# Kernel optimization log

Hardware: AMD Instinct MI355X
Metric: run time of the kernel (lower is better)

Reference implementation:

```python
import jax, jax.numpy as jnp
import numpy as np

KS, PAD = 3, 1  # AttentionConv kernel_size=3, padding=1, stride=1, groups=1


def _unfold(t, H, W):
    # t: [B, C, H+2*PAD, W+2*PAD] -> [B, C, H, W, KS*KS] local windows
    return jnp.stack([t[:, :, i:i + H, j:j + W]
                      for i in range(KS) for j in range(KS)], axis=-1)


def _attn_conv(x, wq, bq, wk, bk, wv, bv, rh, rw):
    # SASA local self-attention conv. x: [B, Cin, H, W]; wq/wk/wv: [Cout, Cin]
    B, Cin, H, W = x.shape
    q = jnp.einsum('bchw,oc->bohw', x, wq) + bq[None, :, None, None]
    xp = jnp.pad(x, ((0, 0), (0, 0), (PAD, PAD), (PAD, PAD)))
    k = jnp.einsum('bchw,oc->bohw', xp, wk) + bk[None, :, None, None]
    v = jnp.einsum('bchw,oc->bohw', xp, wv) + bv[None, :, None, None]
    k = _unfold(k, H, W)  # [B, Cout, H, W, 9]
    v = _unfold(v, H, W)
    Ch = rh.shape[0]  # Cout // 2
    # relative embeddings: first channel half gets rel_h (varies along kh),
    # second half gets rel_w (varies along kw)
    rel = jnp.concatenate([
        jnp.broadcast_to(rh[:, :, None], (Ch, KS, KS)),
        jnp.broadcast_to(rw[:, None, :], (Ch, KS, KS)),
    ], axis=0).reshape(2 * Ch, KS * KS)
    k = k + rel[None, :, None, None, :]
    attn = jax.nn.softmax(q[..., None] * k, axis=-1)  # per-channel softmax over window
    return jnp.einsum('bchwk,bchwk->bchw', attn, v)


def setup_inputs() -> dict:
    key = jax.random.key(0)
    ks = jax.random.split(key, 16)
    B, Cin, Cout = 4, 256, 512
    S, F, O = 64500, 489, 140
    inp = {
        'p3': jax.random.normal(ks[0], (B, Cin, 64, 64), jnp.float32),
        'p4': jax.random.normal(ks[1], (B, Cin, 32, 32), jnp.float32),
        'p5': jax.random.normal(ks[2], (B, Cin, 16, 16), jnp.float32),
        'wq': jax.random.normal(ks[3], (3, Cout, Cin), jnp.float32) * 0.01,
        'bq': jnp.zeros((3, Cout), jnp.float32),
        'wk': jax.random.normal(ks[4], (3, Cout, Cin), jnp.float32) * 0.01,
        'bk': jnp.zeros((3, Cout), jnp.float32),
        'wv': jax.random.normal(ks[5], (3, Cout, Cin), jnp.float32) * 0.01,
        'bv': jnp.zeros((3, Cout), jnp.float32),
        'rel_h': jax.random.normal(ks[6], (3, Cout // 2, KS), jnp.float32),
        'rel_w': jax.random.normal(ks[7], (3, Cout // 2, KS), jnp.float32),
        'ws': jax.random.normal(ks[8], (S, Cout), jnp.float32) * 0.01,
        'bs': jnp.zeros((S,), jnp.float32),
        'wf': jax.random.normal(ks[9], (F, Cout), jnp.float32) * 0.01,
        'bf': jnp.zeros((F,), jnp.float32),
        'wo': jax.random.normal(ks[10], (O, Cout), jnp.float32) * 0.01,
        'bo': jnp.zeros((O,), jnp.float32),
    }
    return inp


def reference(p3, p4, p5, wq, bq, wk, bk, wv, bv, rel_h, rel_w,
              ws, bs, wf, bf, wo, bo):
    feat = 0.
    for i, x in enumerate((p3, p4, p5)):
        y = _attn_conv(x, wq[i], bq[i], wk[i], bk[i], wv[i], bv[i],
                       rel_h[i], rel_w[i])
        y = jax.nn.relu(y)
        feat = feat + y.mean(axis=(2, 3))  # AdaptiveAvgPool2d((1,1)) -> [B, 512]
    # 1x1 conv classifiers on [B, 512, 1, 1] == dense layers; .view(N, -1)
    logits_species = feat @ ws.T + bs
    logits_family = feat @ wf.T + bf
    logits_order = feat @ wo.T + bo
    return (logits_species, logits_family, logits_order)
```

## Files before the change

### kernel.cpp

```cpp
#include <hip/hip_runtime.h>
#include <hip/hip_bf16.h>
#include <stdint.h>

typedef __bf16 bf16x8 __attribute__((ext_vector_type(8)));
typedef float  f32x4  __attribute__((ext_vector_type(4)));
typedef unsigned short u16x8 __attribute__((ext_vector_type(8)));
typedef unsigned int   u32x4 __attribute__((ext_vector_type(4)));

__device__ __forceinline__ unsigned short f2bf(float f) {
    union { float f; unsigned u; } v; v.f = f;
    unsigned r = v.u + 0x7fffu + ((v.u >> 16) & 1u);
    return (unsigned short)(r >> 16);
}
__device__ __forceinline__ float bf2f(unsigned short u) {
    union { unsigned u; float f; } v; v.u = (unsigned)u << 16; return v.f;
}
__device__ __forceinline__ float lo16(unsigned d) {
    union { unsigned u; float f; } v; v.u = d << 16; return v.f;
}
__device__ __forceinline__ float hi16(unsigned d) {
    union { unsigned u; float f; } v; v.u = d & 0xffff0000u; return v.f;
}
__device__ __forceinline__ float fexp2(float x) {
    float r; asm("v_exp_f32 %0, %1" : "=v"(r) : "v"(x)); return r;
}
__device__ __forceinline__ float frcp(float x) {
    float r; asm("v_rcp_f32 %0, %1" : "=v"(r) : "v"(x)); return r;
}

__device__ __forceinline__ void async16(void* lds, const void* g) {
    __builtin_amdgcn_global_load_lds(
        (const __attribute__((address_space(1))) unsigned int*)g,
        (__attribute__((address_space(3))) unsigned int*)lds, 16, 0, 0);
}

#define NT_ALL   21504
#define OFF_L1   16384
#define OFF_L2   20480

__global__ __launch_bounds__(256) void prep_kernel(
    const float* __restrict__ x0, const float* __restrict__ x1,
    const float* __restrict__ x2,
    const float* __restrict__ wq, const float* __restrict__ wk,
    const float* __restrict__ wv,
    unsigned short* __restrict__ wb, unsigned short* __restrict__ xT,
    float* __restrict__ feat)
{
    __shared__ unsigned short tile[64][65];
    int bid = blockIdx.x;
    if (bid == 0) {
        for (int i = threadIdx.x; i < 2048; i += 256) feat[i] = 0.f;
        return;
    }
    bid -= 1;
    if (bid < 576) {
        int t = bid / 192;
        int i = ((bid % 192) * 256 + threadIdx.x) * 8;
        const float* src = (t == 0) ? wq : (t == 1) ? wk : wv;
        f32x4 a = *(const f32x4*)(src + i);
        f32x4 b = *(const f32x4*)(src + i + 4);
        u16x8 o;
        o[0] = f2bf(a.x); o[1] = f2bf(a.y); o[2] = f2bf(a.z); o[3] = f2bf(a.w);
        o[4] = f2bf(b.x); o[5] = f2bf(b.y); o[6] = f2bf(b.z); o[7] = f2bf(b.w);
        *(u16x8*)(wb + (size_t)t * 393216 + i) = o;
        return;
    }
    bid -= 576;
    int xb = bid % 84;
    int c0 = ((bid / 84) & 3) * 64;
    int b  = bid / 336;
    const float* xp; int tb, HW, lvl_off;
    if (xb < 64)      { xp = x0; tb = xb;      HW = 4096; lvl_off = 0;      }
    else if (xb < 80) { xp = x1; tb = xb - 64; HW = 1024; lvl_off = OFF_L1; }
    else              { xp = x2; tb = xb - 80; HW = 256;  lvl_off = OFF_L2; }
    int hw0 = tb * 64;
    xp += (size_t)b * 256 * HW;
    int tx = threadIdx.x & 63;
    int ty = threadIdx.x >> 6;
#pragma unroll
    for (int i = 0; i < 16; ++i) {
        int c = c0 + ty * 16 + i;
        tile[ty * 16 + i][tx] = f2bf(xp[(size_t)c * HW + hw0 + tx]);
    }
    __syncthreads();
    unsigned short* op = xT + ((size_t)lvl_off + (size_t)b * HW + hw0) * 256 + c0;
#pragma unroll
    for (int i = 0; i < 16; ++i) {
        int r = ty * 16 + i;
        op[(size_t)r * 256 + tx] = tile[tx][r];
    }
}

__global__ __launch_bounds__(256, 2) void qkv_gemm_kernel(
    const unsigned short* __restrict__ wb,
    const float* __restrict__ bq, const float* __restrict__ bk,
    const float* __restrict__ bv,
    const unsigned short* __restrict__ xT,
    unsigned short* __restrict__ qkv)
{
    int bid = blockIdx.x;
    int swz = (bid & 7) * 252 + (bid >> 3);
    int nt  = swz / 12;
    int mz  = swz % 12;
    int z   = mz >> 2;
    int bm0 = (mz & 3) * 128;
    int bn0 = nt * 128;
    int lvl = (bn0 >= OFF_L2) ? 2 : (bn0 >= OFF_L1) ? 1 : 0;
    const unsigned short* Wm = wb + ((size_t)z * 3 + lvl) * 131072;
    const float* bias = ((z == 0) ? bq : (z == 1) ? bk : bv) + lvl * 512;
    unsigned short* out = qkv + (size_t)z * 512 * NT_ALL;

    __shared__ unsigned short smem[2][8192];

    int tid  = threadIdx.x;
    int lane = tid & 63;
    int wid  = tid >> 6;
    int wr   = wid >> 1, wc = wid & 1;
    int l15  = lane & 15;
    int kg   = lane >> 4;

    f32x4 acc[4][4];
#pragma unroll
    for (int i = 0; i < 4; ++i)
#pragma unroll
        for (int j = 0; j < 4; ++j) acc[i][j] = (f32x4){0.f, 0.f, 0.f, 0.f};

    int aRow0 = bm0 + (2 * wid)     * 16 + l15;
    int aRow1 = bm0 + (2 * wid + 1) * 16 + l15;
    int bRow0 = bn0 + (2 * wid)     * 16 + l15;
    int bRow1 = bn0 + (2 * wid + 1) * 16 + l15;
    int kbase = kg * 8;

    auto STAGE = [&](int t, int bufi) {
        int kk = t * 32 + kbase;
        unsigned short* As = smem[bufi];
        unsigned short* Bs = As + 4096;
        async16(As + (2 * wid)     * 512, Wm + (size_t)aRow0 * 256 + kk);
        async16(As + (2 * wid + 1) * 512, Wm + (size_t)aRow1 * 256 + kk);
        async16(Bs + (2 * wid)     * 512, xT + (size_t)bRow0 * 256 + kk);
        async16(Bs + (2 * wid + 1) * 512, xT + (size_t)bRow1 * 256 + kk);
    };

    STAGE(0, 0);
    __syncthreads();

    for (int it = 0; it < 8; ++it) {
        if (it < 7) STAGE(it + 1, (it + 1) & 1);
        const unsigned short* As = smem[it & 1];
        const unsigned short* Bs = As + 4096;
        bf16x8 af[4], bg[4];
#pragma unroll
        for (int mi = 0; mi < 4; ++mi)
            af[mi] = *reinterpret_cast<const bf16x8*>(As + ((wr * 4 + mi) * 64 + lane) * 8);
#pragma unroll
        for (int ni = 0; ni < 4; ++ni)
            bg[ni] = *reinterpret_cast<const bf16x8*>(Bs + ((wc * 4 + ni) * 64 + lane) * 8);
#pragma unroll
        for (int mi = 0; mi < 4; ++mi)
#pragma unroll
            for (int ni = 0; ni < 4; ++ni)
                acc[mi][ni] = __builtin_amdgcn_mfma_f32_16x16x32_bf16(
                    af[mi], bg[ni], acc[mi][ni], 0, 0, 0);
        __syncthreads();
    }

    unsigned short* T = smem[0];
#pragma unroll
    for (int p = 0; p < 2; ++p) {
        __syncthreads();
#pragma unroll
        for (int s = 0; s < 2; ++s) {
            int mi = 2 * p + s;
            int qw = wr * 32 + s * 16 + kg * 4;
            int ow = bm0 + wr * 64 + mi * 16 + kg * 4;
#pragma unroll
            for (int ni = 0; ni < 4; ++ni) {
                int cn = wc * 64 + ni * 16 + l15;
#pragma unroll
                for (int r = 0; r < 4; ++r)
                    T[(qw + r) * 136 + cn] = f2bf(acc[mi][ni][r] + bias[ow + r]);
            }
        }
        __syncthreads();
        int q  = tid >> 2;
        int j4 = tid & 3;
        int o  = bm0 + (q >> 5) * 64 + (2 * p + ((q >> 4) & 1)) * 16 + (q & 15);
        unsigned short* orow = out + (size_t)o * NT_ALL + bn0;
#pragma unroll
        for (int c = 0; c < 4; ++c) {
            int nl = c * 32 + j4 * 8;
            *(u16x8*)(orow + nl) = *(const u16x8*)(T + q * 136 + nl);
        }
    }
}

__global__ __launch_bounds__(256, 4) void attn_kernel(
    const unsigned short* __restrict__ qkv,
    const float* __restrict__ bk, const float* __restrict__ bv,
    const float* __restrict__ relh, const float* __restrict__ relw,
    float* __restrict__ feat)
{
    int xb = blockIdx.x;
    int c  = blockIdx.y;
    int lvl, lgW, lvl_off, hw_all;
    if (xb < 8)       { lvl = 0; lgW = 6; lvl_off = 0;      hw_all = xb * 2048 + threadIdx.x * 8; }
    else if (xb < 10) { lvl = 1; lgW = 5; lvl_off = OFF_L1; hw_all = (xb - 8) * 2048 + threadIdx.x * 8; }
    else              { lvl = 2; lgW = 4; lvl_off = OFF_L2; hw_all = threadIdx.x * 8; }
    int W = 1 << lgW, H = W, HW = W << lgW;
    bool active = hw_all < 4 * HW;
    int b  = hw_all >> (2 * lgW);
    int hw = hw_all & (HW - 1);
    int h = hw >> lgW, w0 = hw & (W - 1);

    size_t n0 = (size_t)lvl_off + hw_all;
    const unsigned short* qp = qkv + (size_t)c          * NT_ALL + n0;
    const unsigned short* kp = qkv + ((size_t)512 + c)  * NT_ALL + n0;
    const unsigned short* vp = qkv + ((size_t)1024 + c) * NT_ALL + n0;

    float bkc = bk[lvl * 512 + c], bvc = bv[lvl * 512 + c];
    bool ish = (c < 256);
    const float* rsp = ish ? (relh + lvl * 768 + c * 3)
                           : (relw + lvl * 768 + (c - 256) * 3);
    float rs0 = rsp[0], rs1 = rsp[1], rs2 = rsp[2];

    float ysum = 0.f;
    if (active) {
        float kf[3][10], vf[3][10];
        u32x4 qv = *(const u32x4*)qp;
        float qf[8];
#pragma unroll
        for (int d = 0; d < 4; ++d) { qf[2 * d] = lo16(qv[d]); qf[2 * d + 1] = hi16(qv[d]); }
#pragma unroll
        for (int r = 0; r < 3; ++r) {
            int y = h + r - 1;
            if ((unsigned)y < (unsigned)H) {
                int off = (r - 1) << lgW;
                u32x4 kv = *(const u32x4*)(kp + off);
                u32x4 vv = *(const u32x4*)(vp + off);
#pragma unroll
                for (int d = 0; d < 4; ++d) {
                    kf[r][1 + 2 * d] = lo16(kv[d]); kf[r][2 + 2 * d] = hi16(kv[d]);
                    vf[r][1 + 2 * d] = lo16(vv[d]); vf[r][2 + 2 * d] = hi16(vv[d]);
                }
                bool hasL = (w0 > 0), hasR = (w0 + 8 < W);
                kf[r][0] = hasL ? hi16(*(const unsigned*)(kp + off - 2)) : bkc;
                vf[r][0] = hasL ? hi16(*(const unsigned*)(vp + off - 2)) : bvc;
                kf[r][9] = hasR ? lo16(*(const unsigned*)(kp + off + 8)) : bkc;
                vf[r][9] = hasR ? lo16(*(const unsigned*)(vp + off + 8)) : bvc;
            } else {
#pragma unroll
                for (int j = 0; j < 10; ++j) { kf[r][j] = bkc; vf[r][j] = bvc; }
            }
        }
#define ROW(r, q0, q1, q2)                                         \
        {                                                          \
            float p0 = fexp2(fmaf(qln, kf[r][j + 0], q0));         \
            float p1 = fexp2(fmaf(qln, kf[r][j + 1], q1));         \
            float p2 = fexp2(fmaf(qln, kf[r][j + 2], q2));         \
            num = fmaf(p0, vf[r][j + 0], num);                     \
            num = fmaf(p1, vf[r][j + 1], num);                     \
            num = fmaf(p2, vf[r][j + 2], num);                     \
            den += p0 + p1 + p2;                                   \
        }
        if (ish) {
#pragma unroll
            for (int j = 0; j < 8; ++j) {
                float qln = qf[j] * 1.4426950408889634f;
                float pr0 = qln * rs0, pr1 = qln * rs1, pr2 = qln * rs2;
                float num = 0.f, den = 0.f;
                ROW(0, pr0, pr0, pr0)
                ROW(1, pr1, pr1, pr1)
                ROW(2, pr2, pr2, pr2)
                ysum += fmaxf(num * frcp(den), 0.f);
            }
        } else {
#pragma unroll
            for (int j = 0; j < 8; ++j) {
                float qln = qf[j] * 1.4426950408889634f;
                float pr0 = qln * rs0, pr1 = qln * rs1, pr2 = qln * rs2;
                float num = 0.f, den = 0.f;
                ROW(0, pr0, pr1, pr2)
                ROW(1, pr0, pr1, pr2)
                ROW(2, pr0, pr1, pr2)
                ysum += fmaxf(num * frcp(den), 0.f);
            }
        }
#undef ROW
        ysum *= (1.0f / HW);
    }
#pragma unroll
    for (int off = 16; off; off >>= 1) ysum += __shfl_down(ysum, off, 32);
    if (active && ((threadIdx.x & 31) == 0))
        atomicAdd(&feat[(size_t)b * 512 + c], ysum);
}

__global__ __launch_bounds__(256, 4) void logits_kernel(
    const float* __restrict__ feat,
    const float* __restrict__ ws, const float* __restrict__ bs,
    const float* __restrict__ wf, const float* __restrict__ bff,
    const float* __restrict__ wo, const float* __restrict__ bo,
    float* __restrict__ out)
{
    int lane = threadIdx.x & 63;
    int wid  = threadIdx.x >> 6;
    f32x4 fr[4][2];
#pragma unroll
    for (int b = 0; b < 4; ++b) {
        fr[b][0] = *(const f32x4*)(feat + b * 512 + lane * 4);
        fr[b][1] = *(const f32x4*)(feat + b * 512 + 256 + lane * 4);
    }
    const int ROWS = 64500 + 489 + 140;
    for (int row = blockIdx.x * 4 + wid; row < ROWS; row += 8192) {
        const float* wm; float bias; size_t obase; int ostride;
        if (row < 64500) {
            wm = ws + (size_t)row * 512; bias = bs[row]; obase = (size_t)row; ostride = 64500;
        } else if (row < 64500 + 489) {
            int r = row - 64500;
            wm = wf + (size_t)r * 512; bias = bff[r]; obase = 258000 + (size_t)r; ostride = 489;
        } else {
            int r = row - 64989;
            wm = wo + (size_t)r * 512; bias = bo[r]; obase = 259956 + (size_t)r; ostride = 140;
        }
        f32x4 w1 = *(const f32x4*)(wm + lane * 4);
        f32x4 w2 = *(const f32x4*)(wm + 256 + lane * 4);
        float accs[4];
#pragma unroll
        for (int b = 0; b < 4; ++b) {
            f32x4 f1 = fr[b][0], f2 = fr[b][1];
            accs[b] = w1.x * f1.x + w1.y * f1.y + w1.z * f1.z + w1.w * f1.w
                    + w2.x * f2.x + w2.y * f2.y + w2.z * f2.z + w2.w * f2.w;
        }
#pragma unroll
        for (int off = 32; off; off >>= 1)
#pragma unroll
            for (int b = 0; b < 4; ++b) accs[b] += __shfl_down(accs[b], off, 64);
        if (lane == 0)
#pragma unroll
            for (int b = 0; b < 4; ++b) out[obase + (size_t)b * ostride] = accs[b] + bias;
    }
}

extern "C" void kernel_launch(void* const* d_in, const int* in_sizes, int n_in,
                              void* d_out, int out_size, void* d_ws, size_t ws_size,
                              hipStream_t stream)
{
    const float* x0  = (const float*)d_in[0];
    const float* x1  = (const float*)d_in[1];
    const float* x2  = (const float*)d_in[2];
    const float* wq  = (const float*)d_in[3];
    const float* bq  = (const float*)d_in[4];
    const float* wk  = (const float*)d_in[5];
    const float* bk  = (const float*)d_in[6];
    const float* wv  = (const float*)d_in[7];
    const float* bv  = (const float*)d_in[8];
    const float* relh = (const float*)d_in[9];
    const float* relw = (const float*)d_in[10];
    const float* ws  = (const float*)d_in[11];
    const float* bs  = (const float*)d_in[12];
    const float* wf  = (const float*)d_in[13];
    const float* bff = (const float*)d_in[14];
    const float* wo  = (const float*)d_in[15];
    const float* bo  = (const float*)d_in[16];
    float* out = (float*)d_out;

    char* wsb = (char*)d_ws;
    float* feat = (float*)wsb;
    unsigned short* wb = (unsigned short*)(wsb + 8192);
    unsigned short* xT = (unsigned short*)(wsb + 8192 + 2359296);
    unsigned short* qkv = (unsigned short*)(wsb + 8192 + 2359296 + 11010048);

    prep_kernel<<<dim3(1 + 576 + 1344), 256, 0, stream>>>(
        x0, x1, x2, wq, wk, wv, wb, xT, feat);
    qkv_gemm_kernel<<<dim3(2016), 256, 0, stream>>>(
        wb, bq, bk, bv, xT, qkv);
    attn_kernel<<<dim3(11, 512, 1), 256, 0, stream>>>(
        qkv, bk, bv, relh, relw, feat);
    logits_kernel<<<dim3(2048), 256, 0, stream>>>(feat, ws, bs, wf, bff, wo, bo, out);
}
```

Measured before the change: 134.0 us.

## Halve grid sizes by giving each block two work tiles across all kernels

The prep kernel now converts 16 weights per thread and transposes two input tiles per block. The GEMM processes two N-tiles per block with occupancy hint raised to 4. The attention kernel uses 1024-thread blocks that cover a full level (or levels 1 and 2 together), leaving some threads idle. The logits grid is halved. The aim is to cut block launch and scheduling overhead, at the cost of less parallelism and possible load imbalance or idle lanes.

```diff
diff --git a/kernel.cpp b/kernel.cpp
--- a/kernel.cpp
+++ b/kernel.cpp
@@ -11,9 +11,6 @@
     union { float f; unsigned u; } v; v.f = f;
     unsigned r = v.u + 0x7fffu + ((v.u >> 16) & 1u);
     return (unsigned short)(r >> 16);
-}
-__device__ __forceinline__ float bf2f(unsigned short u) {
-    union { unsigned u; float f; } v; v.u = (unsigned)u << 16; return v.f;
 }
 __device__ __forceinline__ float lo16(unsigned d) {
     union { unsigned u; float f; } v; v.u = d << 16; return v.f;
@@ -53,45 +50,53 @@
         return;
     }
     bid -= 1;
-    if (bid < 576) {
-        int t = bid / 192;
-        int i = ((bid % 192) * 256 + threadIdx.x) * 8;
+    if (bid < 288) {
+        int t = bid / 96;
+        int i = ((bid % 96) * 256 + threadIdx.x) * 16;
         const float* src = (t == 0) ? wq : (t == 1) ? wk : wv;
-        f32x4 a = *(const f32x4*)(src + i);
-        f32x4 b = *(const f32x4*)(src + i + 4);
-        u16x8 o;
-        o[0] = f2bf(a.x); o[1] = f2bf(a.y); o[2] = f2bf(a.z); o[3] = f2bf(a.w);
-        o[4] = f2bf(b.x); o[5] = f2bf(b.y); o[6] = f2bf(b.z); o[7] = f2bf(b.w);
-        *(u16x8*)(wb + (size_t)t * 393216 + i) = o;
+#pragma unroll
+        for (int hh = 0; hh < 2; ++hh) {
+            f32x4 a = *(const f32x4*)(src + i + hh * 8);
+            f32x4 b = *(const f32x4*)(src + i + hh * 8 + 4);
+            u16x8 o;
+            o[0] = f2bf(a.x); o[1] = f2bf(a.y); o[2] = f2bf(a.z); o[3] = f2bf(a.w);
+            o[4] = f2bf(b.x); o[5] = f2bf(b.y); o[6] = f2bf(b.z); o[7] = f2bf(b.w);
+            *(u16x8*)(wb + (size_t)t * 393216 + i + hh * 8) = o;
+        }
         return;
     }
-    bid -= 576;
-    int xb = bid % 84;
-    int c0 = ((bid / 84) & 3) * 64;
-    int b  = bid / 336;
-    const float* xp; int tb, HW, lvl_off;
-    if (xb < 64)      { xp = x0; tb = xb;      HW = 4096; lvl_off = 0;      }
-    else if (xb < 80) { xp = x1; tb = xb - 64; HW = 1024; lvl_off = OFF_L1; }
-    else              { xp = x2; tb = xb - 80; HW = 256;  lvl_off = OFF_L2; }
-    int hw0 = tb * 64;
-    xp += (size_t)b * 256 * HW;
-    int tx = threadIdx.x & 63;
-    int ty = threadIdx.x >> 6;
-#pragma unroll
-    for (int i = 0; i < 16; ++i) {
-        int c = c0 + ty * 16 + i;
-        tile[ty * 16 + i][tx] = f2bf(xp[(size_t)c * HW + hw0 + tx]);
-    }
-    __syncthreads();
-    unsigned short* op = xT + ((size_t)lvl_off + (size_t)b * HW + hw0) * 256 + c0;
-#pragma unroll
-    for (int i = 0; i < 16; ++i) {
-        int r = ty * 16 + i;
-        op[(size_t)r * 256 + tx] = tile[tx][r];
-    }
-}
-
-__global__ __launch_bounds__(256, 2) void qkv_gemm_kernel(
+    bid -= 288;
+    int base = bid * 2;
+    for (int t2 = 0; t2 < 2; ++t2) {
+        int q  = base + t2;
+        int xb = q % 84;
+        int c0 = ((q / 84) & 3) * 64;
+        int b  = q / 336;
+        const float* xp; int tb, HW, lvl_off;
+        if (xb < 64)      { xp = x0; tb = xb;      HW = 4096; lvl_off = 0;      }
+        else if (xb < 80) { xp = x1; tb = xb - 64; HW = 1024; lvl_off = OFF_L1; }
+        else              { xp = x2; tb = xb - 80; HW = 256;  lvl_off = OFF_L2; }
+        int hw0 = tb * 64;
+        const float* xpb = xp + (size_t)b * 256 * HW;
+        int tx = threadIdx.x & 63;
+        int ty = threadIdx.x >> 6;
+        __syncthreads();
+#pragma unroll
+        for (int i = 0; i < 16; ++i) {
+            int c = c0 + ty * 16 + i;
+            tile[ty * 16 + i][tx] = f2bf(xpb[(size_t)c * HW + hw0 + tx]);
+        }
+        __syncthreads();
+        unsigned short* op = xT + ((size_t)lvl_off + (size_t)b * HW + hw0) * 256 + c0;
+#pragma unroll
+        for (int i = 0; i < 16; ++i) {
+            int r = ty * 16 + i;
+            op[(size_t)r * 256 + tx] = tile[tx][r];
+        }
+    }
+}
+
+__global__ __launch_bounds__(256, 4) void qkv_gemm_kernel(
     const unsigned short* __restrict__ wb,
     const float* __restrict__ bq, const float* __restrict__ bk,
     const float* __restrict__ bv,
@@ -99,16 +104,11 @@
     unsigned short* __restrict__ qkv)
 {
     int bid = blockIdx.x;
-    int swz = (bid & 7) * 252 + (bid >> 3);
-    int nt  = swz / 12;
+    int swz = (bid & 7) * 126 + (bid >> 3);
     int mz  = swz % 12;
+    int np  = swz / 12;
     int z   = mz >> 2;
     int bm0 = (mz & 3) * 128;
-    int bn0 = nt * 128;
-    int lvl = (bn0 >= OFF_L2) ? 2 : (bn0 >= OFF_L1) ? 1 : 0;
-    const unsigned short* Wm = wb + ((size_t)z * 3 + lvl) * 131072;
-    const float* bias = ((z == 0) ? bq : (z == 1) ? bk : bv) + lvl * 512;
-    unsigned short* out = qkv + (size_t)z * 512 * NT_ALL;
 
     __shared__ unsigned short smem[2][8192];
 
@@ -118,96 +118,108 @@
     int wr   = wid >> 1, wc = wid & 1;
     int l15  = lane & 15;
     int kg   = lane >> 4;
-
-    f32x4 acc[4][4];
-#pragma unroll
-    for (int i = 0; i < 4; ++i)
-#pragma unroll
-        for (int j = 0; j < 4; ++j) acc[i][j] = (f32x4){0.f, 0.f, 0.f, 0.f};
-
+    int kbase = kg * 8;
     int aRow0 = bm0 + (2 * wid)     * 16 + l15;
     int aRow1 = bm0 + (2 * wid + 1) * 16 + l15;
-    int bRow0 = bn0 + (2 * wid)     * 16 + l15;
-    int bRow1 = bn0 + (2 * wid + 1) * 16 + l15;
-    int kbase = kg * 8;
-
-    auto STAGE = [&](int t, int bufi) {
-        int kk = t * 32 + kbase;
-        unsigned short* As = smem[bufi];
-        unsigned short* Bs = As + 4096;
-        async16(As + (2 * wid)     * 512, Wm + (size_t)aRow0 * 256 + kk);
-        async16(As + (2 * wid + 1) * 512, Wm + (size_t)aRow1 * 256 + kk);
-        async16(Bs + (2 * wid)     * 512, xT + (size_t)bRow0 * 256 + kk);
-        async16(Bs + (2 * wid + 1) * 512, xT + (size_t)bRow1 * 256 + kk);
-    };
-
-    STAGE(0, 0);
-    __syncthreads();
-
-    for (int it = 0; it < 8; ++it) {
-        if (it < 7) STAGE(it + 1, (it + 1) & 1);
-        const unsigned short* As = smem[it & 1];
-        const unsigned short* Bs = As + 4096;
-        bf16x8 af[4], bg[4];
-#pragma unroll
-        for (int mi = 0; mi < 4; ++mi)
-            af[mi] = *reinterpret_cast<const bf16x8*>(As + ((wr * 4 + mi) * 64 + lane) * 8);
-#pragma unroll
-        for (int ni = 0; ni < 4; ++ni)
-            bg[ni] = *reinterpret_cast<const bf16x8*>(Bs + ((wc * 4 + ni) * 64 + lane) * 8);
-#pragma unroll
-        for (int mi = 0; mi < 4; ++mi)
+
+    for (int half = 0; half < 2; ++half) {
+        int nt  = np * 2 + half;
+        int bn0 = nt * 128;
+        int lvl = (bn0 >= OFF_L2) ? 2 : (bn0 >= OFF_L1) ? 1 : 0;
+        const unsigned short* Wm = wb + ((size_t)z * 3 + lvl) * 131072;
+        const float* bias = ((z == 0) ? bq : (z == 1) ? bk : bv) + lvl * 512;
+        unsigned short* out = qkv + (size_t)z * 512 * NT_ALL;
+
+        int bRow0 = bn0 + (2 * wid)     * 16 + l15;
+        int bRow1 = bn0 + (2 * wid + 1) * 16 + l15;
+
+        auto STAGE = [&](int t, int bufi) {
+            int kk = t * 32 + kbase;
+            unsigned short* As = smem[bufi];
+            unsigned short* Bs = As + 4096;
+            async16(As + (2 * wid)     * 512, Wm + (size_t)aRow0 * 256 + kk);
+            async16(As + (2 * wid + 1) * 512, Wm + (size_t)aRow1 * 256 + kk);
+            async16(Bs + (2 * wid)     * 512, xT + (size_t)bRow0 * 256 + kk);
+            async16(Bs + (2 * wid + 1) * 512, xT + (size_t)bRow1 * 256 + kk);
+        };
+
+        f32x4 acc[4][4];
+#pragma unroll
+        for (int i = 0; i < 4; ++i)
+#pragma unroll
+            for (int j = 0; j < 4; ++j) acc[i][j] = (f32x4){0.f, 0.f, 0.f, 0.f};
+
+        __syncthreads();
+        STAGE(0, 0);
+        __syncthreads();
+
+        for (int it = 0; it < 8; ++it) {
+            if (it < 7) STAGE(it + 1, (it + 1) & 1);
+            const unsigned short* As = smem[it & 1];
+            const unsigned short* Bs = As + 4096;
+            bf16x8 af[4], bg[4];
+#pragma unroll
+            for (int mi = 0; mi < 4; ++mi)
+                af[mi] = *reinterpret_cast<const bf16x8*>(As + ((wr * 4 + mi) * 64 + lane) * 8);
 #pragma unroll
             for (int ni = 0; ni < 4; ++ni)
-                acc[mi][ni] = __builtin_amdgcn_mfma_f32_16x16x32_bf16(
-                    af[mi], bg[ni], acc[mi][ni], 0, 0, 0);
-        __syncthreads();
-    }
-
-    unsigned short* T = smem[0];
-#pragma unroll
-    for (int p = 0; p < 2; ++p) {
-        __syncthreads();
-#pragma unroll
-        for (int s = 0; s < 2; ++s) {
-            int mi = 2 * p + s;
-            int qw = wr * 32 + s * 16 + kg * 4;
-            int ow = bm0 + wr * 64 + mi * 16 + kg * 4;
-#pragma unroll
-            for (int ni = 0; ni < 4; ++ni) {
-                int cn = wc * 64 + ni * 16 + l15;
-#pragma unroll
-                for (int r = 0; r < 4; ++r)
-                    T[(qw + r) * 136 + cn] = f2bf(acc[mi][ni][r] + bias[ow + r]);
-            }
-        }
-        __syncthreads();
-        int q  = tid >> 2;
-        int j4 = tid & 3;
-        int o  = bm0 + (q >> 5) * 64 + (2 * p + ((q >> 4) & 1)) * 16 + (q & 15);
-        unsigned short* orow = out + (size_t)o * NT_ALL + bn0;
-#pragma unroll
-        for (int c = 0; c < 4; ++c) {
-            int nl = c * 32 + j4 * 8;
-            *(u16x8*)(orow + nl) = *(const u16x8*)(T + q * 136 + nl);
-        }
-    }
-}
-
-__global__ __launch_bounds__(256, 4) void attn_kernel(
+                bg[ni] = *reinterpret_cast<const bf16x8*>(Bs + ((wc * 4 + ni) * 64 + lane) * 8);
+#pragma unroll
+            for (int mi = 0; mi < 4; ++mi)
+#pragma unroll
+                for (int ni = 0; ni < 4; ++ni)
+                    acc[mi][ni] = __builtin_amdgcn_mfma_f32_16x16x32_bf16(
+                        af[mi], bg[ni], acc[mi][ni], 0, 0, 0);
+            __syncthreads();
+        }
+
+        unsigned short* T = smem[0];
+#pragma unroll
+        for (int p = 0; p < 2; ++p) {
+            __syncthreads();
+#pragma unroll
+            for (int s = 0; s < 2; ++s) {
+                int mi = 2 * p + s;
+                int qw = wr * 32 + s * 16 + kg * 4;
+                int ow = bm0 + wr * 64 + mi * 16 + kg * 4;
+#pragma unroll
+                for (int ni = 0; ni < 4; ++ni) {
+                    int cn = wc * 64 + ni * 16 + l15;
+#pragma unroll
+                    for (int r = 0; r < 4; ++r)
+                        T[(qw + r) * 136 + cn] = f2bf(acc[mi][ni][r] + bias[ow + r]);
+                }
+            }
+            __syncthreads();
+            int q  = tid >> 2;
+            int j4 = tid & 3;
+            int o  = bm0 + (q >> 5) * 64 + (2 * p + ((q >> 4) & 1)) * 16 + (q & 15);
+            unsigned short* orow = out + (size_t)o * NT_ALL + bn0;
+#pragma unroll
+            for (int c = 0; c < 4; ++c) {
+                int nl = c * 32 + j4 * 8;
+                *(u16x8*)(orow + nl) = *(const u16x8*)(T + q * 136 + nl);
+            }
+        }
+    }
+}
+
+__global__ __launch_bounds__(1024, 4) void attn_kernel(
     const unsigned short* __restrict__ qkv,
     const float* __restrict__ bk, const float* __restrict__ bv,
     const float* __restrict__ relh, const float* __restrict__ relw,
     float* __restrict__ feat)
 {
-    int xb = blockIdx.x;
-    int c  = blockIdx.y;
+    int xb  = blockIdx.x;
+    int c   = blockIdx.y;
+    int tid = threadIdx.x;
     int lvl, lgW, lvl_off, hw_all;
-    if (xb < 8)       { lvl = 0; lgW = 6; lvl_off = 0;      hw_all = xb * 2048 + threadIdx.x * 8; }
-    else if (xb < 10) { lvl = 1; lgW = 5; lvl_off = OFF_L1; hw_all = (xb - 8) * 2048 + threadIdx.x * 8; }
-    else              { lvl = 2; lgW = 4; lvl_off = OFF_L2; hw_all = threadIdx.x * 8; }
+    bool active = true;
+    if (xb < 2)         { lvl = 0; lgW = 6; lvl_off = 0;      hw_all = xb * 8192 + tid * 8; }
+    else if (tid < 512) { lvl = 1; lgW = 5; lvl_off = OFF_L1; hw_all = tid * 8; }
+    else                { lvl = 2; lgW = 4; lvl_off = OFF_L2; hw_all = (tid - 512) * 8;
+                          active = (tid - 512) < 128; }
     int W = 1 << lgW, H = W, HW = W << lgW;
-    bool active = hw_all < 4 * HW;
     int b  = hw_all >> (2 * lgW);
     int hw = hw_all & (HW - 1);
     int h = hw >> lgW, w0 = hw & (W - 1);
@@ -290,7 +302,7 @@
     }
 #pragma unroll
     for (int off = 16; off; off >>= 1) ysum += __shfl_down(ysum, off, 32);
-    if (active && ((threadIdx.x & 31) == 0))
+    if (active && ((tid & 31) == 0))
         atomicAdd(&feat[(size_t)b * 512 + c], ysum);
 }
 
@@ -310,7 +322,7 @@
         fr[b][1] = *(const f32x4*)(feat + b * 512 + 256 + lane * 4);
     }
     const int ROWS = 64500 + 489 + 140;
-    for (int row = blockIdx.x * 4 + wid; row < ROWS; row += 8192) {
+    for (int row = blockIdx.x * 4 + wid; row < ROWS; row += 4096) {
         const float* wm; float bias; size_t obase; int ostride;
         if (row < 64500) {
             wm = ws + (size_t)row * 512; bias = bs[row]; obase = (size_t)row; ostride = 64500;
@@ -369,11 +381,11 @@
     unsigned short* xT = (unsigned short*)(wsb + 8192 + 2359296);
     unsigned short* qkv = (unsigned short*)(wsb + 8192 + 2359296 + 11010048);
 
-    prep_kernel<<<dim3(1 + 576 + 1344), 256, 0, stream>>>(
+    prep_kernel<<<dim3(961), 256, 0, stream>>>(
         x0, x1, x2, wq, wk, wv, wb, xT, feat);
-    qkv_gemm_kernel<<<dim3(2016), 256, 0, stream>>>(
+    qkv_gemm_kernel<<<dim3(1008), 256, 0, stream>>>(
         wb, bq, bk, bv, xT, qkv);
-    attn_kernel<<<dim3(11, 512, 1), 256, 0, stream>>>(
+    attn_kernel<<<dim3(3, 512), 1024, 0, stream>>>(
         qkv, bk, bv, relh, relw, feat);
-    logits_kernel<<<dim3(2048), 256, 0, stream>>>(feat, ws, bs, wf, bff, wo, bo, out);
-}
+    logits_kernel<<<dim3(1024), 256, 0, stream>>>(feat, ws, bs, wf, bff, wo, bo, out);
+}
```

Result: slower. 145.5 us (+8.6%).
